# Kernel tuning notes

Measured on AMD Instinct MI355X. Metric: run time of the kernel, lower is better.

Reference implementation:

```python
import jax, jax.numpy as jnp
import numpy as np

NUM_TEAMS = 100000
EMBED = 32
N_EDGES = 2000000
B = 524288
N_CONV = 3
TARGET_DIM = 3


def setup_inputs() -> dict:
    key = jax.random.key(0)
    ks = jax.random.split(key, 20)
    inp = {
        'edge_index': jax.random.randint(ks[0], (2, N_EDGES), 0, NUM_TEAMS),
        'edge_weight': jax.random.uniform(ks[1], (N_EDGES,), dtype=jnp.float32),
        'home': jax.random.randint(ks[2], (B,), 0, NUM_TEAMS),
        'away': jax.random.randint(ks[3], (B,), 0, NUM_TEAMS),
        # embedding table (nn.Embedding(num_teams, embed_dim))
        'embed': jax.random.normal(ks[4], (NUM_TEAMS, EMBED), dtype=jnp.float32) * 0.05,
        # GraphConv params: lin_rel (weight+bias, applied to aggregated msgs) and lin_root (no bias)
        'conv_w_rel': jax.random.normal(ks[5], (N_CONV, 32, 32), dtype=jnp.float32) * 0.1,
        'conv_b_rel': jax.random.normal(ks[6], (N_CONV, 32), dtype=jnp.float32) * 0.01,
        'conv_w_root': jax.random.normal(ks[7], (N_CONV, 32, 32), dtype=jnp.float32) * 0.1,
        # dense stack: 64->8, 8->8, 8->8, 8->8, 8->3
        'lin_w0': jax.random.normal(ks[8], (8, 64), dtype=jnp.float32) * 0.1,
        'lin_b0': jnp.zeros((8,), jnp.float32),
        'lin_w1': jax.random.normal(ks[9], (8, 8), dtype=jnp.float32) * 0.1,
        'lin_b1': jnp.zeros((8,), jnp.float32),
        'lin_w2': jax.random.normal(ks[10], (8, 8), dtype=jnp.float32) * 0.1,
        'lin_b2': jnp.zeros((8,), jnp.float32),
        'lin_w3': jax.random.normal(ks[11], (8, 8), dtype=jnp.float32) * 0.1,
        'lin_b3': jnp.zeros((8,), jnp.float32),
        'lin_w4': jax.random.normal(ks[12], (TARGET_DIM, 8), dtype=jnp.float32) * 0.1,
        'lin_b4': jnp.zeros((TARGET_DIM,), jnp.float32),
    }
    return inp


def _lrelu(x):
    return jax.nn.leaky_relu(x, negative_slope=0.01)


def _graph_conv(x, src, dst, ew, w_rel, b_rel, w_root):
    # PyG GraphConv (aggr='add'): out_i = W_root x_i + W_rel * sum_{j->i} e_ji x_j + b_rel
    msg = x[src] * ew[:, None]                                   # [E, d] gather
    agg = jax.ops.segment_sum(msg, dst, num_segments=NUM_TEAMS)  # [N, d] scatter-add
    return agg @ w_rel.T + b_rel + x @ w_root.T


def reference(edge_index, edge_weight, home, away, embed,
              conv_w_rel, conv_b_rel, conv_w_root,
              lin_w0, lin_b0, lin_w1, lin_b1, lin_w2, lin_b2,
              lin_w3, lin_b3, lin_w4, lin_b4):
    src, dst = edge_index[0], edge_index[1]
    x = embed  # x = embedding(arange(num_teams))
    for i in range(N_CONV):
        x = _lrelu(_graph_conv(x, src, dst, edge_weight,
                               conv_w_rel[i], conv_b_rel[i], conv_w_root[i]))
        # dropout p=0.1 after first conv: identity in eval mode
    h = jnp.concatenate([x[home], x[away]], axis=1)  # [B, 64]
    for w, b in ((lin_w0, lin_b0), (lin_w1, lin_b1), (lin_w2, lin_b2),
                 (lin_w3, lin_b3), (lin_w4, lin_b4)):
        h = _lrelu(h @ w.T + b)  # dropout identity (eval)
    return jax.nn.log_softmax(h, axis=1).reshape(-1, TARGET_DIM)
```

## Files before the change

kernel.cpp:

```cpp
#include <hip/hip_runtime.h>
#include <hip/hip_fp16.h>

#define NUM_TEAMS 100000
#define EMBED     32
#define N_EDGES   2000000
#define BQ        524288
#define TARGET_DIM 3

#define BSH    9
#define BSPAN  512
#define NBUCK  ((NUM_TEAMS + BSPAN - 1) / BSPAN)
#define TILE   8192
#define P2_BLOCKS ((N_EDGES + TILE - 1) / TILE)

__global__ void __launch_bounds__(256) bhist_kernel(const int* __restrict__ dst,
                                                    int* __restrict__ bhist, int n) {
    __shared__ int cnt[NBUCK];
    int t = threadIdx.x;
    for (int i = t; i < NBUCK; i += 256) cnt[i] = 0;
    __syncthreads();
    int base = blockIdx.x * TILE;
    for (int j = 0; j < TILE; j += 256) {
        int i = base + j + t;
        if (i < n) atomicAdd(&cnt[dst[i] >> BSH], 1);
    }
    __syncthreads();
    for (int i = t; i < NBUCK; i += 256) if (cnt[i]) atomicAdd(&bhist[i], cnt[i]);
}

__global__ void __launch_bounds__(256) bscan_kernel(const int* __restrict__ bhist,
                                                    int* __restrict__ bbase,
                                                    int* __restrict__ bcursor,
                                                    int* __restrict__ row_ptr) {
    __shared__ int wsum[4];
    int t = threadIdx.x;
    int v = (t < NBUCK) ? bhist[t] : 0;
    int lane = t & 63, wid = t >> 6;
    int incl = v;
    #pragma unroll
    for (int off = 1; off < 64; off <<= 1) {
        int u = __shfl_up(incl, off, 64);
        if (lane >= off) incl += u;
    }
    if (lane == 63) wsum[wid] = incl;
    __syncthreads();
    int wofs = 0;
    for (int w = 0; w < wid; ++w) wofs += wsum[w];
    int excl = incl - v + wofs;
    if (t < NBUCK) { bbase[t] = excl; bcursor[t] = excl; }
    if (t == 0) { bbase[NBUCK] = N_EDGES; row_ptr[NUM_TEAMS] = N_EDGES; }
}

__global__ void __launch_bounds__(256) partition_kernel(
        const int* __restrict__ src, const int* __restrict__ dst,
        const float* __restrict__ ew,
        int* __restrict__ bcursor, int2* __restrict__ recs, int n) {
    __shared__ int cnt[NBUCK];
    __shared__ int lbase[NBUCK];
    int t = threadIdx.x;
    for (int i = t; i < NBUCK; i += 256) cnt[i] = 0;
    __syncthreads();
    int base = blockIdx.x * TILE;
    for (int j = 0; j < TILE; j += 256) {
        int i = base + j + t;
        if (i < n) atomicAdd(&cnt[dst[i] >> BSH], 1);
    }
    __syncthreads();
    for (int b = t; b < NBUCK; b += 256) {
        int c = cnt[b];
        lbase[b] = c ? atomicAdd(&bcursor[b], c) : 0;
        cnt[b] = 0;
    }
    __syncthreads();
    for (int j = 0; j < TILE; j += 256) {
        int i = base + j + t;
        if (i < n) {
            int d = dst[i];
            int b = d >> BSH;
            int r = atomicAdd(&cnt[b], 1);
            int2 rec;
            rec.x = src[i] | ((d & (BSPAN - 1)) << 17);
            rec.y = __float_as_int(ew[i]);
            recs[lbase[b] + r] = rec;
        }
    }
}

__global__ void __launch_bounds__(256) finalize_kernel(
        const int2* __restrict__ recs, const int* __restrict__ bbase,
        int* __restrict__ row_ptr, int2* __restrict__ epack) {
    __shared__ int cnt[BSPAN];
    __shared__ int excl[BSPAN];
    int b = blockIdx.x;
    int t = threadIdx.x;
    int rbase = bbase[b], rend = bbase[b + 1];
    for (int i = t; i < BSPAN; i += 256) cnt[i] = 0;
    __syncthreads();
    for (int k = rbase + t; k < rend; k += 256)
        atomicAdd(&cnt[recs[k].x >> 17], 1);
    __syncthreads();
    if (t < 64) {
        int c[8]; int s = 0;
        #pragma unroll
        for (int k = 0; k < 8; ++k) { c[k] = cnt[t * 8 + k]; s += c[k]; }
        int incl = s;
        #pragma unroll
        for (int off = 1; off < 64; off <<= 1) {
            int u = __shfl_up(incl, off, 64);
            if (t >= off) incl += u;
        }
        int e = incl - s;
        #pragma unroll
        for (int k = 0; k < 8; ++k) { excl[t * 8 + k] = e; e += c[k]; }
    }
    __syncthreads();
    for (int i = t; i < BSPAN; i += 256) {
        int node = b * BSPAN + i;
        if (node < NUM_TEAMS) row_ptr[node] = rbase + excl[i];
        cnt[i] = excl[i];
    }
    __syncthreads();
    for (int k = rbase + t; k < rend; k += 256) {
        int2 rec = recs[k];
        int dloc = rec.x >> 17;
        int r = atomicAdd(&cnt[dloc], 1);
        int2 e; e.x = rec.x & 0x1FFFF; e.y = rec.y;
        epack[rbase + r] = e;
    }
}

__global__ void __launch_bounds__(256) cvt_kernel(const float* __restrict__ in,
                                                  __half* __restrict__ out, int n2) {
    int i = blockIdx.x * 256 + threadIdx.x;
    if (i < n2) {
        float2 v = *(const float2*)(in + 2 * i);
        *(__half2*)(out + 2 * i) = __floats2half2_rn(v.x, v.y);
    }
}

#define CONV_NPB 16
__global__ void __launch_bounds__(256) conv_kernel(
        const __half* __restrict__ xh,
        const int* __restrict__ row_ptr,
        const int2* __restrict__ epack,
        const float* __restrict__ w_rel,
        const float* __restrict__ b_rel,
        const float* __restrict__ w_root,
        __half* __restrict__ x_out) {
    __shared__ float s_wrelT[32 * 33];
    __shared__ float s_wrootT[32 * 33];
    __shared__ float s_b[32];
    __shared__ float s_agg[CONV_NPB][34];
    __shared__ float s_x[CONV_NPB][34];

    int t = threadIdx.x;
    for (int i = t; i < 1024; i += 256) {
        int j = i >> 5, d = i & 31;
        s_wrelT[d * 33 + j]  = w_rel[i];
        s_wrootT[d * 33 + j] = w_root[i];
    }
    if (t < 32) s_b[t] = b_rel[t];

    int ln = t >> 4;
    int l  = t & 15;
    int node = blockIdx.x * CONV_NPB + ln;

    const __half2* xh2 = (const __half2*)xh;
    float2 xv = __half22float2(xh2[node * 16 + l]);
    int r0 = row_ptr[node], r1 = row_ptr[node + 1];
    int lim = r1 - 1;

    __half2 acc[8];
    #pragma unroll
    for (int j = 0; j < 8; ++j) acc[j] = __floats2half2_rn(0.f, 0.f);

    for (int k = r0; k < r1; k += 8) {
        int sx[8]; float wv[8];
        #pragma unroll
        for (int j = 0; j < 8; ++j) {
            int idx = k + j;
            idx = idx < lim ? idx : lim;
            long long raw = __builtin_nontemporal_load(
                                (const long long*)(epack + idx));
            sx[j] = (int)(unsigned)(raw & 0xffffffffll);
            wv[j] = __int_as_float((int)(raw >> 32));
        }
        __half2 g[8];
        #pragma unroll
        for (int j = 0; j < 8; ++j) g[j] = xh2[sx[j] * 16 + l];
        #pragma unroll
        for (int j = 0; j < 8; ++j) {
            float w = (k + j <= lim) ? wv[j] : 0.f;
            __half2 w2 = __floats2half2_rn(w, w);
            acc[j] = __hfma2(w2, g[j], acc[j]);
        }
    }
    float2 a = {0.f, 0.f};
    #pragma unroll
    for (int j = 0; j < 8; ++j) {
        float2 f = __half22float2(acc[j]);
        a.x += f.x; a.y += f.y;
    }
    *(float2*)&s_agg[ln][2 * l] = a;
    *(float2*)&s_x[ln][2 * l]   = xv;
    __syncthreads();

    int j0 = 2 * l, j1 = 2 * l + 1;
    float o0 = s_b[j0], o1 = s_b[j1];
    #pragma unroll
    for (int d = 0; d < 32; ++d) {
        float ag = s_agg[ln][d];
        float xx = s_x[ln][d];
        o0 += s_wrelT[d * 33 + j0] * ag + s_wrootT[d * 33 + j0] * xx;
        o1 += s_wrelT[d * 33 + j1] * ag + s_wrootT[d * 33 + j1] * xx;
    }
    o0 = (o0 >= 0.f) ? o0 : 0.01f * o0;
    o1 = (o1 >= 0.f) ? o1 : 0.01f * o1;
    ((__half2*)x_out)[node * 16 + l] = __floats2half2_rn(o0, o1);
}

__global__ void __launch_bounds__(256) mlp_kernel(
        const __half* __restrict__ xh,
        const int* __restrict__ home, const int* __restrict__ away,
        const float* __restrict__ w0, const float* __restrict__ b0,
        const float* __restrict__ w1, const float* __restrict__ b1,
        const float* __restrict__ w2, const float* __restrict__ b2,
        const float* __restrict__ w3, const float* __restrict__ b3,
        const float* __restrict__ w4, const float* __restrict__ b4,
        float* __restrict__ out, int n) {
    __shared__ float s_w0[512], s_w1[64], s_w2[64], s_w3[64], s_w4[24];
    __shared__ float s_b0[8], s_b1[8], s_b2[8], s_b3[8], s_b4[3];
    int t = threadIdx.x;
    for (int i = t; i < 512; i += 256) s_w0[i] = w0[i];
    if (t < 64) { s_w1[t] = w1[t]; s_w2[t] = w2[t]; s_w3[t] = w3[t]; }
    if (t < 24) s_w4[t] = w4[t];
    if (t < 8)  { s_b0[t] = b0[t]; s_b1[t] = b1[t]; s_b2[t] = b2[t]; s_b3[t] = b3[t]; }
    if (t < 3)  s_b4[t] = b4[t];
    __syncthreads();

    int i = blockIdx.x * 256 + t;
    if (i >= n) return;

    int hi = __builtin_nontemporal_load(home + i);
    int ai = __builtin_nontemporal_load(away + i);

    float hv[64];
    {
        const __half2* ph = (const __half2*)(xh + (size_t)hi * EMBED);
        const __half2* pa = (const __half2*)(xh + (size_t)ai * EMBED);
        #pragma unroll
        for (int q = 0; q < 16; ++q) {
            float2 f = __half22float2(ph[q]);
            hv[2*q+0] = f.x; hv[2*q+1] = f.y;
        }
        #pragma unroll
        for (int q = 0; q < 16; ++q) {
            float2 f = __half22float2(pa[q]);
            hv[32+2*q+0] = f.x; hv[32+2*q+1] = f.y;
        }
    }

    float h1[8];
    #pragma unroll
    for (int j = 0; j < 8; ++j) {
        float o = s_b0[j];
        #pragma unroll
        for (int d = 0; d < 64; ++d) o += s_w0[j * 64 + d] * hv[d];
        h1[j] = (o >= 0.f) ? o : 0.01f * o;
    }
    float h2[8];
    #pragma unroll
    for (int j = 0; j < 8; ++j) {
        float o = s_b1[j];
        #pragma unroll
        for (int d = 0; d < 8; ++d) o += s_w1[j * 8 + d] * h1[d];
        h2[j] = (o >= 0.f) ? o : 0.01f * o;
    }
    float h3[8];
    #pragma unroll
    for (int j = 0; j < 8; ++j) {
        float o = s_b2[j];
        #pragma unroll
        for (int d = 0; d < 8; ++d) o += s_w2[j * 8 + d] * h2[d];
        h3[j] = (o >= 0.f) ? o : 0.01f * o;
    }
    float h4[8];
    #pragma unroll
    for (int j = 0; j < 8; ++j) {
        float o = s_b3[j];
        #pragma unroll
        for (int d = 0; d < 8; ++d) o += s_w3[j * 8 + d] * h3[d];
        h4[j] = (o >= 0.f) ? o : 0.01f * o;
    }
    float f[3];
    #pragma unroll
    for (int j = 0; j < 3; ++j) {
        float o = s_b4[j];
        #pragma unroll
        for (int d = 0; d < 8; ++d) o += s_w4[j * 8 + d] * h4[d];
        f[j] = (o >= 0.f) ? o : 0.01f * o;
    }
    float m  = fmaxf(f[0], fmaxf(f[1], f[2]));
    float s  = expf(f[0] - m) + expf(f[1] - m) + expf(f[2] - m);
    float ls = logf(s);
    out[3 * i + 0] = f[0] - m - ls;
    out[3 * i + 1] = f[1] - m - ls;
    out[3 * i + 2] = f[2] - m - ls;
}


extern "C" void kernel_launch(void* const* d_in, const int* in_sizes, int n_in,
                              void* d_out, int out_size, void* d_ws, size_t ws_size,
                              hipStream_t stream) {
    const int*   edge_index = (const int*)d_in[0];
    const int*   src   = edge_index;
    const int*   dst   = edge_index + N_EDGES;
    const float* ew    = (const float*)d_in[1];
    const int*   home  = (const int*)d_in[2];
    const int*   away  = (const int*)d_in[3];
    const float* embed = (const float*)d_in[4];
    const float* w_rel  = (const float*)d_in[5];
    const float* b_rel  = (const float*)d_in[6];
    const float* w_root = (const float*)d_in[7];
    const float* w0 = (const float*)d_in[8];  const float* b0 = (const float*)d_in[9];
    const float* w1 = (const float*)d_in[10]; const float* b1 = (const float*)d_in[11];
    const float* w2 = (const float*)d_in[12]; const float* b2 = (const float*)d_in[13];
    const float* w3 = (const float*)d_in[14]; const float* b3 = (const float*)d_in[15];
    const float* w4 = (const float*)d_in[16]; const float* b4 = (const float*)d_in[17];
    float* out = (float*)d_out;

    char* ws = (char*)d_ws;
    size_t off = 0;
    auto carve = [&](size_t bytes) -> void* {
        void* p = ws + off;
        off += (bytes + 255) & ~(size_t)255;
        return p;
    };
    int*   row_ptr = (int*)  carve((NUM_TEAMS + 1) * sizeof(int));
    int*   bhist   = (int*)  carve(NBUCK * sizeof(int));
    int*   bbase   = (int*)  carve((NBUCK + 1) * sizeof(int));
    int*   bcursor = (int*)  carve(NBUCK * sizeof(int));
    int2*  recs    = (int2*) carve((size_t)N_EDGES * sizeof(int2));
    int2*  epack   = (int2*) carve((size_t)N_EDGES * sizeof(int2));
    __half* embedh = (__half*)recs;
    __half* x1h    = (__half*)recs + (size_t)NUM_TEAMS * EMBED;
    __half* x2h    = (__half*)carve((size_t)NUM_TEAMS * EMBED * sizeof(__half));
    (void)ws_size; (void)in_sizes; (void)n_in; (void)out_size;

    const int conv_blocks = NUM_TEAMS / CONV_NPB;
    const int mlp_blocks  = (BQ + 255) / 256;
    const int cvt_pairs   = NUM_TEAMS * EMBED / 2;

    hipMemsetAsync(bhist, 0, NBUCK * sizeof(int), stream);
    bhist_kernel<<<P2_BLOCKS, 256, 0, stream>>>(dst, bhist, N_EDGES);
    bscan_kernel<<<1, 256, 0, stream>>>(bhist, bbase, bcursor, row_ptr);
    partition_kernel<<<P2_BLOCKS, 256, 0, stream>>>(src, dst, ew, bcursor, recs, N_EDGES);
    finalize_kernel<<<NBUCK, 256, 0, stream>>>(recs, bbase, row_ptr, epack);
    cvt_kernel<<<(cvt_pairs + 255) / 256, 256, 0, stream>>>(embed, embedh, cvt_pairs);

    conv_kernel<<<conv_blocks, 256, 0, stream>>>(embedh, row_ptr, epack,
        w_rel + 0 * 1024, b_rel + 0 * 32, w_root + 0 * 1024, x2h);
    conv_kernel<<<conv_blocks, 256, 0, stream>>>(x2h, row_ptr, epack,
        w_rel + 1 * 1024, b_rel + 1 * 32, w_root + 1 * 1024, x1h);
    conv_kernel<<<conv_blocks, 256, 0, stream>>>(x1h, row_ptr, epack,
        w_rel + 2 * 1024, b_rel + 2 * 32, w_root + 2 * 1024, x2h);

    mlp_kernel<<<mlp_blocks, 256, 0, stream>>>(x2h, home, away,
        w0, b0, w1, b1, w2, b2, w3, b3, w4, b4, out, BQ);
}
```

Measured before the change: 267.1 us.

## Precompute per-team first MLP layer projections in last conv to shrink gathers

The first dense layer is linear in the concatenation of the home and away embeddings, so the last conv kernel now computes per-node u = W0[:, :32]·x and v = W0[:, 32:]·x (16 halves) and no longer writes the 32-dim embedding. The MLP kernel gathers 8 halves for each of home and away instead of 32, and its 64-wide dot product becomes an add. This cuts the random-gather traffic and FLOPs in the 524K-row MLP stage, at the cost of a small extra matvec, shared memory and a barrier in the final conv. Rounding u and v to half adds some precision risk.

```diff
diff --git a/kernel.cpp b/kernel.cpp
--- a/kernel.cpp
+++ b/kernel.cpp
@@ -146,12 +146,16 @@
         const float* __restrict__ w_rel,
         const float* __restrict__ b_rel,
         const float* __restrict__ w_root,
-        __half* __restrict__ x_out) {
+        __half* __restrict__ x_out,
+        const float* __restrict__ w0,
+        __half* __restrict__ uv_out) {
     __shared__ float s_wrelT[32 * 33];
     __shared__ float s_wrootT[32 * 33];
     __shared__ float s_b[32];
     __shared__ float s_agg[CONV_NPB][34];
     __shared__ float s_x[CONV_NPB][34];
+    __shared__ float s_o[CONV_NPB][34];
+    __shared__ float s_w0[8 * 66];
 
     int t = threadIdx.x;
     for (int i = t; i < 1024; i += 256) {
@@ -160,6 +164,10 @@
         s_wrootT[d * 33 + j] = w_root[i];
     }
     if (t < 32) s_b[t] = b_rel[t];
+    if (w0) {
+        for (int i = t; i < 512; i += 256)
+            s_w0[(i >> 6) * 66 + (i & 63)] = w0[i];
+    }
 
     int ln = t >> 4;
     int l  = t & 15;
@@ -216,22 +224,32 @@
     }
     o0 = (o0 >= 0.f) ? o0 : 0.01f * o0;
     o1 = (o1 >= 0.f) ? o1 : 0.01f * o1;
-    ((__half2*)x_out)[node * 16 + l] = __floats2half2_rn(o0, o1);
+    if (x_out)
+        ((__half2*)x_out)[node * 16 + l] = __floats2half2_rn(o0, o1);
+
+    if (uv_out) {
+        *(float2*)&s_o[ln][2 * l] = make_float2(o0, o1);
+        __syncthreads();
+        const float* wrow = (l < 8) ? (s_w0 + l * 66) : (s_w0 + (l - 8) * 66 + 32);
+        float uvv = 0.f;
+        #pragma unroll
+        for (int d = 0; d < 32; ++d) uvv += wrow[d] * s_o[ln][d];
+        uv_out[node * 16 + l] = __float2half(uvv);
+    }
 }
 
 __global__ void __launch_bounds__(256) mlp_kernel(
-        const __half* __restrict__ xh,
+        const __half* __restrict__ uv,
         const int* __restrict__ home, const int* __restrict__ away,
-        const float* __restrict__ w0, const float* __restrict__ b0,
+        const float* __restrict__ b0,
         const float* __restrict__ w1, const float* __restrict__ b1,
         const float* __restrict__ w2, const float* __restrict__ b2,
         const float* __restrict__ w3, const float* __restrict__ b3,
         const float* __restrict__ w4, const float* __restrict__ b4,
         float* __restrict__ out, int n) {
-    __shared__ float s_w0[512], s_w1[64], s_w2[64], s_w3[64], s_w4[24];
+    __shared__ float s_w1[64], s_w2[64], s_w3[64], s_w4[24];
     __shared__ float s_b0[8], s_b1[8], s_b2[8], s_b3[8], s_b4[3];
     int t = threadIdx.x;
-    for (int i = t; i < 512; i += 256) s_w0[i] = w0[i];
     if (t < 64) { s_w1[t] = w1[t]; s_w2[t] = w2[t]; s_w3[t] = w3[t]; }
     if (t < 24) s_w4[t] = w4[t];
     if (t < 8)  { s_b0[t] = b0[t]; s_b1[t] = b1[t]; s_b2[t] = b2[t]; s_b3[t] = b3[t]; }
@@ -244,30 +262,20 @@
     int hi = __builtin_nontemporal_load(home + i);
     int ai = __builtin_nontemporal_load(away + i);
 
-    float hv[64];
-    {
-        const __half2* ph = (const __half2*)(xh + (size_t)hi * EMBED);
-        const __half2* pa = (const __half2*)(xh + (size_t)ai * EMBED);
-        #pragma unroll
-        for (int q = 0; q < 16; ++q) {
-            float2 f = __half22float2(ph[q]);
-            hv[2*q+0] = f.x; hv[2*q+1] = f.y;
-        }
-        #pragma unroll
-        for (int q = 0; q < 16; ++q) {
-            float2 f = __half22float2(pa[q]);
-            hv[32+2*q+0] = f.x; hv[32+2*q+1] = f.y;
-        }
-    }
+    const __half2* pu = (const __half2*)(uv + (size_t)hi * 16);
+    const __half2* pv = (const __half2*)(uv + (size_t)ai * 16 + 8);
 
     float h1[8];
     #pragma unroll
-    for (int j = 0; j < 8; ++j) {
-        float o = s_b0[j];
-        #pragma unroll
-        for (int d = 0; d < 64; ++d) o += s_w0[j * 64 + d] * hv[d];
-        h1[j] = (o >= 0.f) ? o : 0.01f * o;
-    }
+    for (int q = 0; q < 4; ++q) {
+        float2 fu = __half22float2(pu[q]);
+        float2 fv = __half22float2(pv[q]);
+        float o0 = fu.x + fv.x + s_b0[2 * q];
+        float o1 = fu.y + fv.y + s_b0[2 * q + 1];
+        h1[2 * q]     = (o0 >= 0.f) ? o0 : 0.01f * o0;
+        h1[2 * q + 1] = (o1 >= 0.f) ? o1 : 0.01f * o1;
+    }
+
     float h2[8];
     #pragma unroll
     for (int j = 0; j < 8; ++j) {
@@ -345,6 +353,7 @@
     __half* embedh = (__half*)recs;
     __half* x1h    = (__half*)recs + (size_t)NUM_TEAMS * EMBED;
     __half* x2h    = (__half*)carve((size_t)NUM_TEAMS * EMBED * sizeof(__half));
+    __half* uv     = (__half*)carve((size_t)NUM_TEAMS * 16 * sizeof(__half));
     (void)ws_size; (void)in_sizes; (void)n_in; (void)out_size;
 
     const int conv_blocks = NUM_TEAMS / CONV_NPB;
@@ -359,12 +368,12 @@
     cvt_kernel<<<(cvt_pairs + 255) / 256, 256, 0, stream>>>(embed, embedh, cvt_pairs);
 
     conv_kernel<<<conv_blocks, 256, 0, stream>>>(embedh, row_ptr, epack,
-        w_rel + 0 * 1024, b_rel + 0 * 32, w_root + 0 * 1024, x2h);
+        w_rel + 0 * 1024, b_rel + 0 * 32, w_root + 0 * 1024, x2h, nullptr, nullptr);
     conv_kernel<<<conv_blocks, 256, 0, stream>>>(x2h, row_ptr, epack,
-        w_rel + 1 * 1024, b_rel + 1 * 32, w_root + 1 * 1024, x1h);
+        w_rel + 1 * 1024, b_rel + 1 * 32, w_root + 1 * 1024, x1h, nullptr, nullptr);
     conv_kernel<<<conv_blocks, 256, 0, stream>>>(x1h, row_ptr, epack,
-        w_rel + 2 * 1024, b_rel + 2 * 32, w_root + 2 * 1024, x2h);
-
-    mlp_kernel<<<mlp_blocks, 256, 0, stream>>>(x2h, home, away,
-        w0, b0, w1, b1, w2, b2, w3, b3, w4, b4, out, BQ);
-}
+        w_rel + 2 * 1024, b_rel + 2 * 32, w_root + 2 * 1024, nullptr, w0, uv);
+
+    mlp_kernel<<<mlp_blocks, 256, 0, stream>>>(uv, home, away,
+        b0, w1, b1, w2, b2, w3, b3, w4, b4, out, BQ);
+}
```

Measured after the change: 251.3 us. 5.9% less time.
